# Kernel tuning notes

Hardware: AMD Instinct MI355X
Metric: run time of the kernel (lower is better)

## Reference

```python
import jax, jax.numpy as jnp
import numpy as np

N = 16000; E = 256000; K = 4000; H = 4; D = 128; CL = 16
NODE_VOCAB = 512; TASK_VOCAB = 128; NEG = 0.2


def _gat_sparse(h_in, src, dst, W, a_s, a_d, b):
    # PyG GATConv, heads=H, concat=False, eval mode (attention dropout off)
    n = h_in.shape[0]
    h = (h_in @ W.T).reshape(n, H, D)                       # [N,H,D]
    e = jax.nn.leaky_relu((h * a_s).sum(-1)[src] + (h * a_d).sum(-1)[dst], NEG)  # [E,H]
    emax = jax.ops.segment_max(e, dst, num_segments=n)
    ex = jnp.exp(e - emax[dst])
    den = jax.ops.segment_sum(ex, dst, num_segments=n)
    alpha = ex / (den[dst] + 1e-16)                         # edge softmax over dst
    out = jax.ops.segment_sum(h[src] * alpha[:, :, None], dst, num_segments=n)
    return out.mean(axis=1) + b                             # mean over heads + bias


def reference(x, edge_index, batch, task, node_emb, task_emb,
              W1, as1, ad1, b1, W2, as2, ad2, b2, W3, as3, ad3, b3,
              sag_wrel, sag_brel, sag_wroot, dmon_w, dmon_b,
              Wt, att_s_t, att_d_t, bt, gate_w, gate_b, trans_w, trans_b,
              task_w, task_b, fuse_w, fuse_b, out_w, out_b):
    src0, dst0 = edge_index[0], edge_index[1]
    loops = jnp.arange(N, dtype=src0.dtype)                 # GATConv add_self_loops=True
    src = jnp.concatenate([src0, loops]); dst = jnp.concatenate([dst0, loops])
    h = node_emb[x]
    h = jax.nn.relu(_gat_sparse(h, src, dst, W1, as1, ad1, b1))
    h = jax.nn.relu(_gat_sparse(h, src, dst, W2, as2, ad2, b2))
    h = jax.nn.relu(_gat_sparse(h, src, dst, W3, as3, ad3, b3))
    # SAGPooling: GraphConv score (add-aggr) + top-k (single graph, k=K), tanh gating
    agg = jax.ops.segment_sum(h[src0], dst0, num_segments=N)
    score = (agg @ sag_wrel.T + sag_brel + h @ sag_wroot.T)[:, 0]
    vals, perm = jax.lax.top_k(score, K)
    xp = h[perm] * jnp.tanh(vals)[:, None]                  # [K,D]
    # filter_adj + to_dense_adj: dense [K,K] adjacency among kept nodes (adj[src,dst]+=1)
    new_idx = jnp.full((N,), -1, jnp.int32).at[perm].set(jnp.arange(K, dtype=jnp.int32))
    ni, nj = new_idx[src0], new_idx[dst0]
    valid = (ni >= 0) & (nj >= 0)
    adj = jnp.zeros((K + 1, K + 1), xp.dtype).at[
        jnp.where(valid, ni, K), jnp.where(valid, nj, K)].add(1.0)[:K, :K]
    dx, adj = xp[None], adj[None]                           # [1,K,D], [1,K,K]; mask all-true
    # DMoNPooling
    s = jax.nn.softmax(dx @ dmon_w.T + dmon_b, axis=-1)     # [1,K,CL]
    out_x = jax.nn.selu(jnp.einsum('bnc,bnf->bcf', s, dx))  # [1,CL,D]
    out_adj = jnp.einsum('bnc,bnm,bmd->bcd', s, adj, s)     # [1,CL,CL]
    deg = adj.sum(axis=1)[..., None]                        # einsum('ijk->ik'): [1,K,1]
    m = deg.sum(axis=(1, 2)) / 2
    ca = jnp.einsum('bnc,bnl->bcl', s, deg)                 # [1,CL,1]
    cb = jnp.einsum('bln,bnc->blc', jnp.swapaxes(deg, 1, 2), s)  # [1,1,CL]
    spectral = (-jnp.trace(out_adj - ca @ cb / 2 / m[:, None, None], axis1=1, axis2=2) / 2 / m).mean()
    ss = jnp.einsum('bnc,bnd->bcd', s, s)
    i_s = jnp.eye(CL, dtype=ss.dtype)
    ortho = jnp.linalg.norm(ss / jnp.linalg.norm(ss, axis=(1, 2), keepdims=True)
                            - i_s / jnp.sqrt(jnp.asarray(CL, ss.dtype)), axis=(1, 2)).mean()
    cluster = (jnp.linalg.norm(s.sum(axis=1), axis=1) / K * jnp.sqrt(jnp.asarray(CL, ss.dtype)) - 1).mean()
    gp_loss = spectral + ortho + cluster
    out_adj = out_adj * (1.0 - i_s)                         # zero diagonal
    ds = jnp.sqrt(out_adj.sum(axis=2)) + 1e-15              # [1,CL]
    out_adj = out_adj / ds[:, None, :] / ds[:, :, None]
    # DenseGATConv (add_loop=True sets diag to 1; adj only used as a mask)
    hh = (out_x @ Wt.T).reshape(1, CL, H, D)
    al = jax.nn.leaky_relu((hh * att_s_t).sum(-1)[:, None, :, :]
                           + (hh * att_d_t).sum(-1)[:, :, None, :], NEG)  # [1,i,j,H]
    adj_l = out_adj * (1.0 - i_s) + i_s
    al = jnp.where(adj_l[..., None] == 0, -jnp.inf, al)
    al = jax.nn.softmax(al, axis=2)
    dg = jax.nn.relu(jnp.einsum('bijh,bjhd->bihd', al, hh).mean(axis=2) + bt)  # [1,CL,D]
    # gated readout (DenseAggregation)
    gate = jax.nn.softmax((dg @ gate_w.T + gate_b)[..., 0], axis=-1)           # [1,CL]
    ro = jnp.einsum('bn,bnd->bd', gate, dg @ trans_w.T + trans_b)              # [1,D]
    te = jax.nn.relu(task_emb[task] @ task_w.T + task_b)                       # [1,D]
    fuse = jax.nn.relu(jnp.concatenate([ro, te], axis=-1) @ fuse_w.T + fuse_b)
    out = fuse @ out_w.T + out_b                                               # [1,1]
    return out, gp_loss


def setup_inputs() -> dict:
    key = jax.random.key(0)
    ks = iter(jax.random.split(key, 64))
    def nrm(shape, scale=0.05):
        return jax.random.normal(next(ks), shape, jnp.float32) * scale
    inp = {}
    inp['x'] = jax.random.randint(next(ks), (N,), 0, NODE_VOCAB, dtype=jnp.int32)
    src = jax.random.randint(next(ks), (E,), 0, N, dtype=jnp.int32)
    off = jax.random.randint(next(ks), (E,), 1, N, dtype=jnp.int32)
    inp['edge_index'] = jnp.stack([src, (src + off) % N])  # no self-loops
    inp['batch'] = jnp.zeros((N,), jnp.int32)
    inp['task'] = jax.random.randint(next(ks), (1,), 0, TASK_VOCAB, dtype=jnp.int32)
    inp['node_emb'] = nrm((NODE_VOCAB, D), D ** -0.5)
    inp['task_emb'] = nrm((TASK_VOCAB, D), D ** -0.5)
    for i in (1, 2, 3):
        inp[f'W{i}'] = nrm((H * D, D)); inp[f'as{i}'] = nrm((H, D))
        inp[f'ad{i}'] = nrm((H, D)); inp[f'b{i}'] = jnp.zeros((D,), jnp.float32)
    inp['sag_wrel'] = nrm((1, D)); inp['sag_brel'] = jnp.zeros((1,), jnp.float32)
    inp['sag_wroot'] = nrm((1, D))
    inp['dmon_w'] = nrm((CL, D)); inp['dmon_b'] = jnp.zeros((CL,), jnp.float32)
    inp['Wt'] = nrm((H * D, D)); inp['att_s_t'] = nrm((H, D)); inp['att_d_t'] = nrm((H, D))
    inp['bt'] = jnp.zeros((D,), jnp.float32)
    inp['gate_w'] = nrm((1, D)); inp['gate_b'] = jnp.zeros((1,), jnp.float32)
    inp['trans_w'] = nrm((D, D)); inp['trans_b'] = jnp.zeros((D,), jnp.float32)
    inp['task_w'] = nrm((D, D)); inp['task_b'] = jnp.zeros((D,), jnp.float32)
    inp['fuse_w'] = nrm((D, 2 * D)); inp['fuse_b'] = jnp.zeros((D,), jnp.float32)
    inp['out_w'] = nrm((1, D)); inp['out_b'] = jnp.zeros((1,), jnp.float32)
    return inp
```

## Files before the change

kernel.cpp:

```cpp
#include <hip/hip_runtime.h>
#include <hip/hip_bf16.h>
#include <math.h>

constexpr int NN  = 16000;
constexpr int NE  = 256000;
constexpr int NET = NE + NN;
constexpr int NK  = 4000;
constexpr int NCL = 16;

constexpr int A_ADJ    = 0;
constexpr int A_SS     = 256;
constexpr int A_CSUM   = 512;
constexpr int A_V      = 528;
constexpr int A_DEGSUM = 544;
constexpr int A_OUTX   = 560;
constexpr int ACC_FLOATS = 3072;

typedef short sh8 __attribute__((ext_vector_type(8)));
typedef float f32x4 __attribute__((ext_vector_type(4)));

__device__ inline unsigned fkey(float f){
  unsigned u = __float_as_uint(f);
  return (u & 0x80000000u) ? ~u : (u | 0x80000000u);
}
__device__ inline unsigned short f2bf(float f){
  unsigned u = __float_as_uint(f);
  unsigned r = u + 0x7FFFu + ((u>>16)&1u);
  return (unsigned short)(r>>16);
}
__device__ inline float bflo(unsigned v){ return __uint_as_float(v<<16); }
__device__ inline float bfhi(unsigned v){ return __uint_as_float(v & 0xFFFF0000u); }

__global__ __launch_bounds__(256) void k_init(int* cnt, int* node2k, float* tbuf,
                       float* deg, float* acc,
                       const float* __restrict__ dw, unsigned short* __restrict__ dwb,
                       const float* __restrict__ W0, const float* __restrict__ as0, const float* __restrict__ ad0,
                       const float* __restrict__ W1, const float* __restrict__ as1, const float* __restrict__ ad1,
                       const float* __restrict__ W2, const float* __restrict__ as2, const float* __restrict__ ad2,
                       const float* __restrict__ Wt, unsigned short* __restrict__ Wtb,
                       float* __restrict__ usd, unsigned short* __restrict__ Blay){
  int i = blockIdx.x*blockDim.x + threadIdx.x;
  int stride = gridDim.x*blockDim.x;
  for (int j=i; j<NN; j+=stride){ cnt[j]=0; node2k[j]=-1; }
  for (int j=i; j<NK*NCL; j+=stride) tbuf[j]=0.f;
  for (int j=i; j<NK; j+=stride) deg[j]=0.f;
  for (int j=i; j<ACC_FLOATS; j+=stride) acc[j]=0.f;
  int b = blockIdx.x;
  const float* Wl[3] = {W0, W1, W2};
  const float* al_s[3] = {as0, as1, as2};
  const float* al_d[3] = {ad0, ad1, ad2};
  if (b < 96){
    int layer = b>>5;
    const float* W = Wl[layer];
    int idx = (b&31)*256 + threadIdx.x;
    int lane = idx&63, kc = (idx>>6)&15, c = idx>>10;
    int d = c*16 + (lane&15), q = lane>>4;
    sh8 v;
    #pragma unroll
    for (int j=0;j<8;j++){
      int kkg = kc*32 + q*8 + j;
      int h = kkg>>7, k = kkg&127;
      v[j] = (short)f2bf(W[(size_t)(h*128+d)*128 + k]);
    }
    *((sh8*)(Blay + (size_t)layer*65536 + (size_t)idx*8)) = v;
  } else if (b < 99){
    int layer = b-96;
    const float* W = Wl[layer];
    const float* as_ = al_s[layer];
    const float* ad_ = al_d[layer];
    for (int t2 = threadIdx.x; t2 < 512; t2 += 256){
      int h = t2>>7, k = t2&127;
      float ss=0.f, sd=0.f;
      for (int d=0; d<128; d++){
        float w = W[(size_t)(h*128+d)*128 + k];
        ss += as_[h*128+d]*w;
        sd += ad_[h*128+d]*w;
      }
      usd[layer*1024 + t2] = ss;
      usd[layer*1024 + 512 + t2] = sd;
    }
  } else if (b == 99){
    int idx = threadIdx.x;
    int kc = idx>>6, lane = idx&63;
    int c = lane&15, q = lane>>4;
    sh8 v;
    #pragma unroll
    for (int j=0;j<8;j++) v[j] = (short)f2bf(dw[(size_t)c*128 + kc*32 + q*8 + j]);
    ((sh8*)dwb)[idx] = v;
  } else if (b < 132){
    int idx = (b-100)*256 + threadIdx.x;
    int lane = idx&63, kc = (idx>>6)&3, ntile = idx>>8;
    int o = ntile*16 + (lane&15), q = lane>>4;
    sh8 v;
    #pragma unroll
    for (int j=0;j<8;j++) v[j] = (short)f2bf(Wt[(size_t)o*128 + kc*32 + q*8 + j]);
    ((sh8*)Wtb)[idx] = v;
  }
}

__global__ void k_count(const int* __restrict__ ei, int* __restrict__ cnt){
  int e = blockIdx.x*blockDim.x + threadIdx.x;
  if (e >= NET) return;
  int d = (e < NE) ? ei[NE+e] : (e-NE);
  atomicAdd(&cnt[d], 1);
}

__global__ __launch_bounds__(1024) void k_scan(int* cnt, int* ptr, int* fill){
  __shared__ int sums[1024];
  int t = threadIdx.x;
  constexpr int PER = 16;
  int base = t*PER;
  int v[PER];
  int run = 0;
  #pragma unroll
  for (int i=0;i<PER;i++){
    int idx = base+i;
    int c = (idx<NN)? cnt[idx] : 0;
    v[i] = run; run += c;
  }
  sums[t] = run;
  __syncthreads();
  for (int o=1;o<1024;o<<=1){
    int add = (t>=o)? sums[t-o] : 0;
    __syncthreads();
    sums[t] += add;
    __syncthreads();
  }
  int ex = sums[t] - run;
  #pragma unroll
  for (int i=0;i<PER;i++){
    int idx = base+i;
    if (idx<NN){ int p = ex+v[i]; ptr[idx]=p; fill[idx]=p; }
  }
  if (t==1023) ptr[NN]=sums[1023];
}

__global__ void k_fill(const int* __restrict__ ei, int* cur, int* csrc){
  int e = blockIdx.x*blockDim.x + threadIdx.x;
  if (e >= NET) return;
  int s, d;
  if (e < NE){ s = ei[e]; d = ei[NE+e]; } else { s = e-NE; d = e-NE; }
  int pos = atomicAdd(&cur[d], 1);
  csrc[pos] = s;
}

__global__ __launch_bounds__(64) void k_embsum(const int* __restrict__ x,
    const float* __restrict__ emb, const float* __restrict__ usd,
    unsigned short* __restrict__ hbf, float* __restrict__ sum_s,
    float* __restrict__ sum_d){
  int n = blockIdx.x, lane = threadIdx.x;
  int xv = x[n];
  float2 v = *(const float2*)&emb[(size_t)xv*128 + 2*lane];
  *(ushort2*)&hbf[(size_t)n*128 + 2*lane] = (ushort2){f2bf(v.x), f2bf(v.y)};
  float ps[4], pd[4];
  #pragma unroll
  for (int h=0;h<4;h++){
    float2 us = *(const float2*)&usd[h*128 + 2*lane];
    float2 ud = *(const float2*)&usd[512 + h*128 + 2*lane];
    ps[h] = v.x*us.x + v.y*us.y;
    pd[h] = v.x*ud.x + v.y*ud.y;
  }
  #pragma unroll
  for (int o=32;o>0;o>>=1){
    #pragma unroll
    for (int h=0;h<4;h++){ ps[h]+=__shfl_down(ps[h],o); pd[h]+=__shfl_down(pd[h],o); }
  }
  if (lane==0){
    ((float4*)sum_s)[n] = (float4){ps[0],ps[1],ps[2],ps[3]};
    ((float4*)sum_d)[n] = (float4){pd[0],pd[1],pd[2],pd[3]};
  }
}

__global__ __launch_bounds__(64) void k_edgeagg(const int* __restrict__ ptr,
    const int* __restrict__ csrc,
    const float* __restrict__ sum_s, const float* __restrict__ sum_d,
    const unsigned short* __restrict__ hbf, unsigned short* __restrict__ agg){
  __shared__ float alf[64*4];
  __shared__ int   sN[64];
  int n = blockIdx.x; int lane = threadIdx.x;
  int b0 = ptr[n], b1 = ptr[n+1];
  int deg = b1 - b0;
  float4 sd = ((const float4*)sum_d)[n];
  bool act = lane < deg;
  int s0i = -1;
  float vx=-1e30f, vy=-1e30f, vz=-1e30f, vw=-1e30f;
  if (act){
    s0i = csrc[b0+lane];
    float4 ss = ((const float4*)sum_s)[s0i];
    vx = ss.x+sd.x; vx = vx>0.f? vx : 0.2f*vx;
    vy = ss.y+sd.y; vy = vy>0.f? vy : 0.2f*vy;
    vz = ss.z+sd.z; vz = vz>0.f? vz : 0.2f*vz;
    vw = ss.w+sd.w; vw = vw>0.f? vw : 0.2f*vw;
  }
  float mx=vx, my=vy, mz=vz, mw=vw;
  for (int base=64; base<deg; base+=64){
    int j = b0+base+lane;
    if (j<b1){
      float4 ss = ((const float4*)sum_s)[csrc[j]];
      float t0=ss.x+sd.x; t0=t0>0.f?t0:0.2f*t0; mx=fmaxf(mx,t0);
      float t1=ss.y+sd.y; t1=t1>0.f?t1:0.2f*t1; my=fmaxf(my,t1);
      float t2=ss.z+sd.z; t2=t2>0.f?t2:0.2f*t2; mz=fmaxf(mz,t2);
      float t3=ss.w+sd.w; t3=t3>0.f?t3:0.2f*t3; mw=fmaxf(mw,t3);
    }
  }
  #pragma unroll
  for (int o=1;o<64;o<<=1){
    mx=fmaxf(mx,__shfl_xor(mx,o)); my=fmaxf(my,__shfl_xor(my,o));
    mz=fmaxf(mz,__shfl_xor(mz,o)); mw=fmaxf(mw,__shfl_xor(mw,o));
  }
  float dx = act? __expf(vx-mx):0.f, dy = act? __expf(vy-my):0.f;
  float dz = act? __expf(vz-mz):0.f, dw = act? __expf(vw-mw):0.f;
  for (int base=64; base<deg; base+=64){
    int j = b0+base+lane;
    if (j<b1){
      float4 ss = ((const float4*)sum_s)[csrc[j]];
      float t0=ss.x+sd.x; t0=t0>0.f?t0:0.2f*t0; dx+=__expf(t0-mx);
      float t1=ss.y+sd.y; t1=t1>0.f?t1:0.2f*t1; dy+=__expf(t1-my);
      float t2=ss.z+sd.z; t2=t2>0.f?t2:0.2f*t2; dz+=__expf(t2-mz);
      float t3=ss.w+sd.w; t3=t3>0.f?t3:0.2f*t3; dw+=__expf(t3-mw);
    }
  }
  #pragma unroll
  for (int o=1;o<64;o<<=1){
    dx+=__shfl_xor(dx,o); dy+=__shfl_xor(dy,o);
    dz+=__shfl_xor(dz,o); dw+=__shfl_xor(dw,o);
  }
  float scx = 0.25f/(dx+1e-16f), scy = 0.25f/(dy+1e-16f);
  float scz = 0.25f/(dz+1e-16f), scw = 0.25f/(dw+1e-16f);
  float a00=0.f,a01=0.f,a10=0.f,a11=0.f,a20=0.f,a21=0.f,a30=0.f,a31=0.f;
  for (int base=0; base<deg; base+=64){
    if (base){
      __syncthreads();
      int j = b0+base+lane;
      if (j<b1){
        s0i = csrc[j];
        float4 ss = ((const float4*)sum_s)[s0i];
        vx=ss.x+sd.x; vx=vx>0.f?vx:0.2f*vx;
        vy=ss.y+sd.y; vy=vy>0.f?vy:0.2f*vy;
        vz=ss.z+sd.z; vz=vz>0.f?vz:0.2f*vz;
        vw=ss.w+sd.w; vw=vw>0.f?vw:0.2f*vw;
      }
    }
    if (base+lane < deg){
      alf[lane*4+0]=__expf(vx-mx)*scx; alf[lane*4+1]=__expf(vy-my)*scy;
      alf[lane*4+2]=__expf(vz-mz)*scz; alf[lane*4+3]=__expf(vw-mw)*scw;
      sN[lane]=s0i;
    }
    __syncthreads();
    int m = deg-base; if (m>64) m=64;
    int e=0;
    for (; e+4<=m; e+=4){
      int t0=sN[e], t1=sN[e+1], t2=sN[e+2], t3=sN[e+3];
      float4 A0=*(float4*)&alf[e*4],   A1=*(float4*)&alf[e*4+4];
      float4 A2=*(float4*)&alf[e*4+8], A3=*(float4*)&alf[e*4+12];
      unsigned g0=*(const unsigned*)&hbf[(size_t)t0*128+2*lane];
      unsigned g1=*(const unsigned*)&hbf[(size_t)t1*128+2*lane];
      unsigned g2=*(const unsigned*)&hbf[(size_t)t2*128+2*lane];
      unsigned g3=*(const unsigned*)&hbf[(size_t)t3*128+2*lane];
      float p0=bflo(g0), p1=bfhi(g0);
      a00+=A0.x*p0; a01+=A0.x*p1; a10+=A0.y*p0; a11+=A0.y*p1;
      a20+=A0.z*p0; a21+=A0.z*p1; a30+=A0.w*p0; a31+=A0.w*p1;
      p0=bflo(g1); p1=bfhi(g1);
      a00+=A1.x*p0; a01+=A1.x*p1; a10+=A1.y*p0; a11+=A1.y*p1;
      a20+=A1.z*p0; a21+=A1.z*p1; a30+=A1.w*p0; a31+=A1.w*p1;
      p0=bflo(g2); p1=bfhi(g2);
      a00+=A2.x*p0; a01+=A2.x*p1; a10+=A2.y*p0; a11+=A2.y*p1;
      a20+=A2.z*p0; a21+=A2.z*p1; a30+=A2.w*p0; a31+=A2.w*p1;
      p0=bflo(g3); p1=bfhi(g3);
      a00+=A3.x*p0; a01+=A3.x*p1; a10+=A3.y*p0; a11+=A3.y*p1;
      a20+=A3.z*p0; a21+=A3.z*p1; a30+=A3.w*p0; a31+=A3.w*p1;
    }
    for (; e<m; e++){
      int t0=sN[e];
      float4 A0=*(float4*)&alf[e*4];
      unsigned g0=*(const unsigned*)&hbf[(size_t)t0*128+2*lane];
      float p0=bflo(g0), p1=bfhi(g0);
      a00+=A0.x*p0; a01+=A0.x*p1; a10+=A0.y*p0; a11+=A0.y*p1;
      a20+=A0.z*p0; a21+=A0.z*p1; a30+=A0.w*p0; a31+=A0.w*p1;
    }
  }
  unsigned short* o = agg + (size_t)n*512;
  *(ushort2*)&o[      2*lane] = (ushort2){f2bf(a00), f2bf(a01)};
  *(ushort2*)&o[128 + 2*lane] = (ushort2){f2bf(a10), f2bf(a11)};
  *(ushort2*)&o[256 + 2*lane] = (ushort2){f2bf(a20), f2bf(a21)};
  *(ushort2*)&o[384 + 2*lane] = (ushort2){f2bf(a30), f2bf(a31)};
}

__global__ __launch_bounds__(256) void k_gemmb(const unsigned short* __restrict__ A,
      const unsigned short* __restrict__ B, const float* __restrict__ bias,
      float* __restrict__ C, unsigned short* __restrict__ Cb, int writeF32,
      int mode, const float* __restrict__ usdn,
      const float* __restrict__ wrel, const float* __restrict__ wroot,
      float* __restrict__ sum_s, float* __restrict__ sum_d,
      float* __restrict__ pbuf, float* __restrict__ qbuf){
  __shared__ float U[1024];
  int tid = threadIdx.x;
  if (mode==0){
    for (int i=tid;i<1024;i+=256) U[i]=usdn[i];
  } else {
    if (tid<128) U[tid]=wrel[tid];
    else if (tid<256) U[tid]=wroot[tid-128];
  }
  __syncthreads();
  int w = tid>>6, lane = tid&63;
  int m0 = blockIdx.x*64 + w*16;
  int quad = lane>>4, col16 = lane&15;
  int mrow = m0 + col16;
  const sh8* arow = (const sh8*)(A + (size_t)mrow*512 + quad*8);
  sh8 af[16];
  #pragma unroll
  for (int kc=0;kc<16;kc++) af[kc] = arow[kc*4];
  f32x4 acc[8];
  #pragma unroll
  for (int c=0;c<8;c++) acc[c] = (f32x4){0.f,0.f,0.f,0.f};
  const sh8* bp = (const sh8*)B;
  #pragma unroll
  for (int kc=0;kc<16;kc++){
    #pragma unroll
    for (int c=0;c<8;c++){
      sh8 bf = bp[(c*16+kc)*64 + lane];
      acc[c] = __builtin_amdgcn_mfma_f32_16x16x32_bf16(af[kc], bf, acc[c], 0, 0, 0);
    }
  }
  float br[8];
  #pragma unroll
  for (int c=0;c<8;c++) br[c] = bias[c*16+col16];
  #pragma unroll
  for (int r=0;r<4;r++){
    int m = m0 + quad*4 + r;
    float vv[8];
    #pragma unroll
    for (int c=0;c<8;c++){
      vv[c] = fmaxf(acc[c][r] + br[c], 0.f);
      Cb[(size_t)m*128 + c*16+col16] = f2bf(vv[c]);
      if (writeF32) C[(size_t)m*128 + c*16+col16] = vv[c];
    }
    if (mode==0){
      float p0=0,p1=0,p2=0,p3=0,q0=0,q1=0,q2=0,q3=0;
      #pragma unroll
      for (int c=0;c<8;c++){
        int o = c*16+col16;
        float val = vv[c];
        p0+=val*U[o];     p1+=val*U[128+o]; p2+=val*U[256+o]; p3+=val*U[384+o];
        q0+=val*U[512+o]; q1+=val*U[640+o]; q2+=val*U[768+o]; q3+=val*U[896+o];
      }
      #pragma unroll
      for (int o2=1;o2<16;o2<<=1){
        p0+=__shfl_xor(p0,o2); p1+=__shfl_xor(p1,o2); p2+=__shfl_xor(p2,o2); p3+=__shfl_xor(p3,o2);
        q0+=__shfl_xor(q0,o2); q1+=__shfl_xor(q1,o2); q2+=__shfl_xor(q2,o2); q3+=__shfl_xor(q3,o2);
      }
      if (col16==0){
        ((float4*)sum_s)[m] = (float4){p0,p1,p2,p3};
        ((float4*)sum_d)[m] = (float4){q0,q1,q2,q3};
      }
    } else {
      float pp=0.f, qq=0.f;
      #pragma unroll
      for (int c=0;c<8;c++){
        int o = c*16+col16;
        pp += vv[c]*U[o]; qq += vv[c]*U[128+o];
      }
      #pragma unroll
      for (int o2=1;o2<16;o2<<=1){ pp+=__shfl_xor(pp,o2); qq+=__shfl_xor(qq,o2); }
      if (col16==0){ pbuf[m]=pp; qbuf[m]=qq; }
    }
  }
}

__global__ __launch_bounds__(64) void k_sagw(const int* __restrict__ ptr,
                           const int* __restrict__ csrc,
                           const float* __restrict__ p, const float* __restrict__ q,
                           const float* __restrict__ brel, float* __restrict__ score){
  int n = blockIdx.x; int lane = threadIdx.x;
  int b0=ptr[n], b1=ptr[n+1];
  float s=0.f;
  for (int j=b0+lane; j<b1; j+=64){
    int sj=csrc[j];
    if (sj!=n) s+=p[sj];
  }
  #pragma unroll
  for (int o=32;o>0;o>>=1) s += __shfl_down(s,o);
  if (lane==0) score[n] = s + q[n] + brel[0];
}

__global__ __launch_bounds__(1024) void k_topk(const float* __restrict__ score,
                                               int* __restrict__ sel){
  __shared__ int hist[8*257];
  __shared__ int hmerge[256];
  __shared__ unsigned sh_prefix;
  __shared__ int sh_rem;
  __shared__ int cntGT, cntEQ;
  __shared__ int ties[256];
  int t = threadIdx.x;
  int lane = t & 63;
  int rep = t >> 7;
  unsigned keys[16];
  #pragma unroll
  for (int j=0;j<16;j++){
    int i = t + j*1024;
    keys[j] = (i<NN) ? fkey(score[i]) : 0u;
  }
  if (t==0){ sh_prefix=0u; sh_rem=NK; cntGT=0; cntEQ=0; }
  __syncthreads();
  for (int p=0;p<4;p++){
    int shift = 24-8*p;
    for (int i=t;i<8*257;i+=1024) hist[i]=0;
    __syncthreads();
    unsigned prefix = sh_prefix;
    #pragma unroll
    for (int j=0;j<16;j++){
      bool val = (j<15) || (t < (NN - 15*1024));
      unsigned u = keys[j];
      bool ok = val && ((p==0) || ((u>>(shift+8)) == (prefix>>(shift+8))));
      int b = (int)((u>>shift)&255u);
      unsigned long long act = __ballot(ok);
      if (act){
        int leader = (int)(__ffsll((long long)act)-1);
        int bl = __shfl(b, leader);
        unsigned long long same = __ballot(ok && b==bl);
        if (same==act){
          if (lane==leader) atomicAdd(&hist[rep*257+bl], (int)__popcll(act));
        } else if (ok){
          atomicAdd(&hist[rep*257+b], 1);
        }
      }
    }
    __syncthreads();
    if (t<256){
      int v=0;
      #pragma unroll
      for (int r=0;r<8;r++) v += hist[r*257+t];
      hmerge[t]=v;
    }
    __syncthreads();
    if (t<64){
      int l = t;
      int b0 = 4*(63-l);
      int c3 = hmerge[b0+3], c2 = hmerge[b0+2], c1 = hmerge[b0+1], c0 = hmerge[b0];
      int gs = c0+c1+c2+c3;
      int incl = gs;
      #pragma unroll
      for (int o=1;o<64;o<<=1){
        int v = __shfl_up(incl, o);
        if (l>=o) incl += v;
      }
      int excl = incl - gs;
      int rem = sh_rem;
      int rl = rem - excl;
      if (rl > 0 && rl <= gs){
        unsigned pre = sh_prefix;
        if (rl > c3){ rl -= c3;
          if (rl > c2){ rl -= c2;
            if (rl > c1){ rl -= c1;
              sh_prefix = pre | ((unsigned)b0<<shift);     sh_rem = rl;
            } else { sh_prefix = pre | ((unsigned)(b0+1)<<shift); sh_rem = rl; }
          } else { sh_prefix = pre | ((unsigned)(b0+2)<<shift);   sh_rem = rl; }
        } else { sh_prefix = pre | ((unsigned)(b0+3)<<shift);     sh_rem = rl; }
      }
    }
    __syncthreads();
  }
  unsigned Tu = sh_prefix;
  #pragma unroll
  for (int j=0;j<16;j++){
    int i = t + j*1024;
    bool val = (i<NN);
    unsigned u = keys[j];
    bool g = val && (u>Tu), e = val && (u==Tu);
    unsigned long long mg = __ballot(g);
    if (mg){
      int leader = (int)(__ffsll((long long)mg)-1);
      int base = 0;
      if (lane==leader) base = atomicAdd(&cntGT, (int)__popcll(mg));
      base = __shfl(base, leader);
      if (g){
        int pos = base + (int)__popcll(mg & ((1ull<<lane)-1ull));
        sel[pos] = i;
      }
    }
    unsigned long long me = __ballot(e);
    if (me){
      int leader = (int)(__ffsll((long long)me)-1);
      int base = 0;
      if (lane==leader) base = atomicAdd(&cntEQ, (int)__popcll(me));
      base = __shfl(base, leader);
      if (e){
        int pos = base + (int)__popcll(me & ((1ull<<lane)-1ull));
        if (pos<256) ties[pos] = i;
      }
    }
  }
  __syncthreads();
  if (t==0){
    int base=cntGT, rem=sh_rem, nt=min(cntEQ,256);
    for (int r=0;r<rem;r++){
      int best=0x7fffffff, bi=-1;
      for (int q2=0;q2<nt;q2++){ int v=ties[q2]; if (v>=0 && v<best){best=v;bi=q2;} }
      sel[base+r] = (bi>=0)? best : 0;
      if (bi>=0) ties[bi]=-1;
    }
  }
}

__global__ __launch_bounds__(256) void k_gassign(const int* __restrict__ sel,
                          const float* __restrict__ score,
                          const float* __restrict__ h, float* __restrict__ xp,
// ... 242 lines not shown
    }
  }
  __syncthreads();
  {
    int w = t>>6, lane = t&63;
    int quad = lane>>4, col = lane&15;
    sh8 af2[2];
    #pragma unroll
    for (int kc=0;kc<2;kc++) af2[kc] = *(const sh8*)&albf[col*64 + kc*32 + quad*8];
    #pragma unroll
    for (int nt2=0; nt2<2; nt2++){
      int ntile = w*2 + nt2;
      int d = ntile*16 + col;
      f32x4 a2 = (f32x4){0.f,0.f,0.f,0.f};
      #pragma unroll
      for (int kc=0;kc<2;kc++){
        sh8 bf;
        #pragma unroll
        for (int j2=0;j2<8;j2++){
          int k = kc*32 + quad*8 + j2;
          int h2 = k>>4, jj = k&15;
          bf[j2] = (short)hhb[jj*512 + h2*128 + d];
        }
        a2 = __builtin_amdgcn_mfma_f32_16x16x32_bf16(af2[kc], bf, a2, 0, 0, 0);
      }
      float bd = bt[d];
      #pragma unroll
      for (int r=0;r<4;r++){
        int i = quad*4 + r;
        dg[i*128 + d] = fmaxf(0.25f*a2[r] + bd, 0.f);
      }
    }
  }
  __syncthreads();
  if (t<16){
    float s=0.f;
    const float4* d4 = (const float4*)&dg[t*128];
    const float4* g4 = (const float4*)gate_w;
    #pragma unroll
    for (int k2=0;k2<32;k2++){
      float4 a = d4[k2], b = g4[k2];
      s += a.x*b.x + a.y*b.y + a.z*b.z + a.w*b.w;
    }
    red[t] = s + gate_b[0];
  }
  __syncthreads();
  if (t<16){
    float mx=-1e30f; for (int i=0;i<16;i++) mx=fmaxf(mx,red[i]);
    float s=0.f; for (int i=0;i<16;i++) s+=__expf(red[i]-mx);
    gate[t]=__expf(red[t]-mx)/s;
  }
  __syncthreads();
  if (t<128){
    float s=0.f;
    for (int i=0;i<16;i++) s += gate[i]*dg[i*128+t];
    gvec[t]=s;
  }
  __syncthreads();
  if (t<128){
    float s=0.f;
    const float4* tw = (const float4*)(trans_w + (size_t)t*128);
    const float4* gv = (const float4*)gvec;
    #pragma unroll
    for (int k2=0;k2<32;k2++){
      float4 a = gv[k2], b = tw[k2];
      s += a.x*b.x + a.y*b.y + a.z*b.z + a.w*b.w;
    }
    ro[t]=s+trans_b[t];
    int tk = task[0];
    const float4* te4 = (const float4*)(task_emb + (size_t)tk*128);
    const float4* tw2 = (const float4*)(task_w + (size_t)t*128);
    float s2=0.f;
    #pragma unroll
    for (int k2=0;k2<32;k2++){
      float4 a = te4[k2], b = tw2[k2];
      s2 += a.x*b.x + a.y*b.y + a.z*b.z + a.w*b.w;
    }
    te[t]=fmaxf(s2+task_b[t],0.f);
  }
  __syncthreads();
  if (t<128){
    float s=0.f;
    const float4* fw = (const float4*)(fuse_w + (size_t)t*256);
    const float4* ro4 = (const float4*)ro;
    const float4* te4 = (const float4*)te;
    #pragma unroll
    for (int k2=0;k2<32;k2++){
      float4 a = ro4[k2], b = fw[k2];
      s += a.x*b.x + a.y*b.y + a.z*b.z + a.w*b.w;
    }
    #pragma unroll
    for (int k2=0;k2<32;k2++){
      float4 a = te4[k2], b = fw[32+k2];
      s += a.x*b.x + a.y*b.y + a.z*b.z + a.w*b.w;
    }
    fu[t]=fmaxf(s+fuse_b[t],0.f);
  }
  __syncthreads();
  float v = (t<128)? fu[t]*out_w[t] : 0.f;
  red[t]=v; __syncthreads();
  for (int o=128;o>0;o>>=1){ if (t<o) red[t]+=red[t+o]; __syncthreads(); }
  if (t==0) dout[0]=red[0]+out_b[0];
}

extern "C" void kernel_launch(void* const* d_in, const int* in_sizes, int n_in,
                              void* d_out, int out_size, void* d_ws, size_t ws_size,
                              hipStream_t stream){
  const int* x        = (const int*)d_in[0];
  const int* ei       = (const int*)d_in[1];
  const int* task     = (const int*)d_in[3];
  const float* node_emb = (const float*)d_in[4];
  const float* task_emb = (const float*)d_in[5];
  const float* W[3]  = {(const float*)d_in[6],  (const float*)d_in[10], (const float*)d_in[14]};
  const float* As_[3]= {(const float*)d_in[7],  (const float*)d_in[11], (const float*)d_in[15]};
  const float* Ad_[3]= {(const float*)d_in[8],  (const float*)d_in[12], (const float*)d_in[16]};
  const float* Bb[3] = {(const float*)d_in[9],  (const float*)d_in[13], (const float*)d_in[17]};
  const float* wrel  = (const float*)d_in[18];
  const float* brel  = (const float*)d_in[19];
  const float* wroot = (const float*)d_in[20];
  const float* dmon_w= (const float*)d_in[21];
  const float* dmon_b= (const float*)d_in[22];
  const float* Wt    = (const float*)d_in[23];
  const float* att_s = (const float*)d_in[24];
  const float* att_d = (const float*)d_in[25];
  const float* btb   = (const float*)d_in[26];
  const float* gate_w= (const float*)d_in[27];
  const float* gate_b= (const float*)d_in[28];
  const float* trans_w=(const float*)d_in[29];
  const float* trans_b=(const float*)d_in[30];
  const float* task_w= (const float*)d_in[31];
  const float* task_b= (const float*)d_in[32];
  const float* fuse_w= (const float*)d_in[33];
  const float* fuse_b= (const float*)d_in[34];
  const float* out_w = (const float*)d_in[35];
  const float* out_b = (const float*)d_in[36];
  float* dout = (float*)d_out;
  (void)in_sizes; (void)n_in; (void)out_size; (void)ws_size;

  char* base = (char*)d_ws;
  size_t off = 0;
  auto alloc = [&](size_t bytes)->char*{
    off = (off + 255) & ~(size_t)255;
    char* r = base + off; off += bytes; return r;
  };
  int* csr_ptr  = (int*)alloc((size_t)(NN+1)*4);
  int* csr_fill = (int*)alloc((size_t)NN*4);
  int* csr_src  = (int*)alloc((size_t)NET*4);
  int* sel      = (int*)alloc((size_t)NK*4);
  int* node2k   = (int*)alloc((size_t)NN*4);
  float* score  = (float*)alloc((size_t)NN*4);
  float* pbuf   = (float*)alloc((size_t)NN*4);
  float* qbuf   = (float*)alloc((size_t)NN*4);
  float* h_a    = (float*)alloc((size_t)NN*128*4);
  unsigned short* hbf  = (unsigned short*)alloc((size_t)NN*128*2);
  unsigned short* aggb = (unsigned short*)alloc((size_t)NN*512*2);
  unsigned short* blay = (unsigned short*)alloc((size_t)3*65536*2);
  unsigned short* dwb  = (unsigned short*)alloc((size_t)256*8*2);
  unsigned short* wtb  = (unsigned short*)alloc((size_t)65536*2);
  float* usd    = (float*)alloc((size_t)3*1024*4);
  float* sum_s  = (float*)alloc((size_t)NN*4*4);
  float* sum_d  = (float*)alloc((size_t)NN*4*4);
  float* xp     = (float*)alloc((size_t)NK*128*4);
  float* sA     = (float*)alloc((size_t)NK*16*4);
  float* tbuf   = (float*)alloc((size_t)NK*16*4);
  float* deg    = (float*)alloc((size_t)NK*4);
  float* acc    = (float*)alloc((size_t)ACC_FLOATS*4);

  k_init<<<256, 256, 0, stream>>>(csr_fill, node2k, tbuf, deg, acc, dmon_w, dwb,
                                  W[0], As_[0], Ad_[0], W[1], As_[1], Ad_[1],
                                  W[2], As_[2], Ad_[2], Wt, wtb, usd, blay);
  k_count<<<(NET+255)/256, 256, 0, stream>>>(ei, csr_fill);
  k_scan<<<1, 1024, 0, stream>>>(csr_fill, csr_ptr, csr_fill);
  k_fill<<<(NET+255)/256, 256, 0, stream>>>(ei, csr_fill, csr_src);
  k_embsum<<<NN, 64, 0, stream>>>(x, node_emb, usd, hbf, sum_s, sum_d);

  for (int l=0;l<3;l++){
    k_edgeagg<<<NN, 64, 0, stream>>>(csr_ptr, csr_src, sum_s, sum_d, hbf, aggb);
    if (l<2){
      k_gemmb<<<NN/64, 256, 0, stream>>>(aggb, blay + (size_t)l*65536, Bb[l],
                                         h_a, hbf, 0, 0, usd + (l+1)*1024,
                                         nullptr, nullptr, sum_s, sum_d,
                                         nullptr, nullptr);
    } else {
      k_gemmb<<<NN/64, 256, 0, stream>>>(aggb, blay + (size_t)2*65536, Bb[2],
                                         h_a, hbf, 1, 1, nullptr,
                                         wrel, wroot, nullptr, nullptr,
                                         pbuf, qbuf);
    }
  }
  k_sagw<<<NN, 64, 0, stream>>>(csr_ptr, csr_src, pbuf, qbuf, brel, score);
  k_topk<<<1, 1024, 0, stream>>>(score, sel);
  k_gassign<<<NK/16, 256, 0, stream>>>(sel, score, h_a, xp, node2k, dwb, dmon_b, sA);
  k_edgepool<<<(NE+255)/256, 256, 0, stream>>>(ei, node2k, sA, tbuf, deg);
  k_pool<<<P_BLOCKS, 256, 0, stream>>>(sA, xp, tbuf, deg, acc);
  k_tail<<<1, 256, 0, stream>>>(acc, wtb, att_s, att_d, btb, gate_w, gate_b,
                                trans_w, trans_b, task, task_emb, task_w, task_b,
                                fuse_w, fuse_b, out_w, out_b, dout);
}
```

Before: 413.5 us.

## Fuse GAT edge aggregation into per-layer MFMA GEMM kernel via LDS staging

Merges the per-node attention softmax/aggregation kernel with the following bf16 MFMA projection GEMM. Each 256-thread block aggregates 64 nodes into shared memory and then runs the GEMM from LDS, which removes the global write and read of the 16000x512 aggregate buffer. The node features and attention sums now ping-pong between two buffers to avoid read/write races across blocks. Attention weights are broadcast with wave shuffles instead of LDS. The trade-off is far fewer blocks (250) with serial 16-node loops per wave and a large LDS footprint, which reduces the latency hiding available to the irregular gather.

```diff
diff --git a/kernel.cpp b/kernel.cpp
--- a/kernel.cpp
+++ b/kernel.cpp
@@ -171,145 +171,142 @@
   }
 }
 
-__global__ __launch_bounds__(64) void k_edgeagg(const int* __restrict__ ptr,
-    const int* __restrict__ csrc,
-    const float* __restrict__ sum_s, const float* __restrict__ sum_d,
-    const unsigned short* __restrict__ hbf, unsigned short* __restrict__ agg){
-  __shared__ float alf[64*4];
-  __shared__ int   sN[64];
-  int n = blockIdx.x; int lane = threadIdx.x;
-  int b0 = ptr[n], b1 = ptr[n+1];
-  int deg = b1 - b0;
-  float4 sd = ((const float4*)sum_d)[n];
-  bool act = lane < deg;
-  int s0i = -1;
-  float vx=-1e30f, vy=-1e30f, vz=-1e30f, vw=-1e30f;
-  if (act){
-    s0i = csrc[b0+lane];
-    float4 ss = ((const float4*)sum_s)[s0i];
-    vx = ss.x+sd.x; vx = vx>0.f? vx : 0.2f*vx;
-    vy = ss.y+sd.y; vy = vy>0.f? vy : 0.2f*vy;
-    vz = ss.z+sd.z; vz = vz>0.f? vz : 0.2f*vz;
-    vw = ss.w+sd.w; vw = vw>0.f? vw : 0.2f*vw;
-  }
-  float mx=vx, my=vy, mz=vz, mw=vw;
-  for (int base=64; base<deg; base+=64){
-    int j = b0+base+lane;
-    if (j<b1){
-      float4 ss = ((const float4*)sum_s)[csrc[j]];
-      float t0=ss.x+sd.x; t0=t0>0.f?t0:0.2f*t0; mx=fmaxf(mx,t0);
-      float t1=ss.y+sd.y; t1=t1>0.f?t1:0.2f*t1; my=fmaxf(my,t1);
-      float t2=ss.z+sd.z; t2=t2>0.f?t2:0.2f*t2; mz=fmaxf(mz,t2);
-      float t3=ss.w+sd.w; t3=t3>0.f?t3:0.2f*t3; mw=fmaxf(mw,t3);
-    }
-  }
-  #pragma unroll
-  for (int o=1;o<64;o<<=1){
-    mx=fmaxf(mx,__shfl_xor(mx,o)); my=fmaxf(my,__shfl_xor(my,o));
-    mz=fmaxf(mz,__shfl_xor(mz,o)); mw=fmaxf(mw,__shfl_xor(mw,o));
-  }
-  float dx = act? __expf(vx-mx):0.f, dy = act? __expf(vy-my):0.f;
-  float dz = act? __expf(vz-mz):0.f, dw = act? __expf(vw-mw):0.f;
-  for (int base=64; base<deg; base+=64){
-    int j = b0+base+lane;
-    if (j<b1){
-      float4 ss = ((const float4*)sum_s)[csrc[j]];
-      float t0=ss.x+sd.x; t0=t0>0.f?t0:0.2f*t0; dx+=__expf(t0-mx);
-      float t1=ss.y+sd.y; t1=t1>0.f?t1:0.2f*t1; dy+=__expf(t1-my);
-      float t2=ss.z+sd.z; t2=t2>0.f?t2:0.2f*t2; dz+=__expf(t2-mz);
-      float t3=ss.w+sd.w; t3=t3>0.f?t3:0.2f*t3; dw+=__expf(t3-mw);
-    }
-  }
-  #pragma unroll
-  for (int o=1;o<64;o<<=1){
-    dx+=__shfl_xor(dx,o); dy+=__shfl_xor(dy,o);
-    dz+=__shfl_xor(dz,o); dw+=__shfl_xor(dw,o);
-  }
-  float scx = 0.25f/(dx+1e-16f), scy = 0.25f/(dy+1e-16f);
-  float scz = 0.25f/(dz+1e-16f), scw = 0.25f/(dw+1e-16f);
-  float a00=0.f,a01=0.f,a10=0.f,a11=0.f,a20=0.f,a21=0.f,a30=0.f,a31=0.f;
-  for (int base=0; base<deg; base+=64){
-    if (base){
-      __syncthreads();
-      int j = b0+base+lane;
-      if (j<b1){
-        s0i = csrc[j];
-        float4 ss = ((const float4*)sum_s)[s0i];
-        vx=ss.x+sd.x; vx=vx>0.f?vx:0.2f*vx;
-        vy=ss.y+sd.y; vy=vy>0.f?vy:0.2f*vy;
-        vz=ss.z+sd.z; vz=vz>0.f?vz:0.2f*vz;
-        vw=ss.w+sd.w; vw=vw>0.f?vw:0.2f*vw;
-      }
-    }
-    if (base+lane < deg){
-      alf[lane*4+0]=__expf(vx-mx)*scx; alf[lane*4+1]=__expf(vy-my)*scy;
-      alf[lane*4+2]=__expf(vz-mz)*scz; alf[lane*4+3]=__expf(vw-mw)*scw;
-      sN[lane]=s0i;
-    }
-    __syncthreads();
-    int m = deg-base; if (m>64) m=64;
-    int e=0;
-    for (; e+4<=m; e+=4){
-      int t0=sN[e], t1=sN[e+1], t2=sN[e+2], t3=sN[e+3];
-      float4 A0=*(float4*)&alf[e*4],   A1=*(float4*)&alf[e*4+4];
-      float4 A2=*(float4*)&alf[e*4+8], A3=*(float4*)&alf[e*4+12];
-      unsigned g0=*(const unsigned*)&hbf[(size_t)t0*128+2*lane];
-      unsigned g1=*(const unsigned*)&hbf[(size_t)t1*128+2*lane];
-      unsigned g2=*(const unsigned*)&hbf[(size_t)t2*128+2*lane];
-      unsigned g3=*(const unsigned*)&hbf[(size_t)t3*128+2*lane];
-      float p0=bflo(g0), p1=bfhi(g0);
-      a00+=A0.x*p0; a01+=A0.x*p1; a10+=A0.y*p0; a11+=A0.y*p1;
-      a20+=A0.z*p0; a21+=A0.z*p1; a30+=A0.w*p0; a31+=A0.w*p1;
-      p0=bflo(g1); p1=bfhi(g1);
-      a00+=A1.x*p0; a01+=A1.x*p1; a10+=A1.y*p0; a11+=A1.y*p1;
-      a20+=A1.z*p0; a21+=A1.z*p1; a30+=A1.w*p0; a31+=A1.w*p1;
-      p0=bflo(g2); p1=bfhi(g2);
-      a00+=A2.x*p0; a01+=A2.x*p1; a10+=A2.y*p0; a11+=A2.y*p1;
-      a20+=A2.z*p0; a21+=A2.z*p1; a30+=A2.w*p0; a31+=A2.w*p1;
-      p0=bflo(g3); p1=bfhi(g3);
-      a00+=A3.x*p0; a01+=A3.x*p1; a10+=A3.y*p0; a11+=A3.y*p1;
-      a20+=A3.z*p0; a21+=A3.z*p1; a30+=A3.w*p0; a31+=A3.w*p1;
-    }
-    for (; e<m; e++){
-      int t0=sN[e];
-      float4 A0=*(float4*)&alf[e*4];
-      unsigned g0=*(const unsigned*)&hbf[(size_t)t0*128+2*lane];
-      float p0=bflo(g0), p1=bfhi(g0);
-      a00+=A0.x*p0; a01+=A0.x*p1; a10+=A0.y*p0; a11+=A0.y*p1;
-      a20+=A0.z*p0; a21+=A0.z*p1; a30+=A0.w*p0; a31+=A0.w*p1;
-    }
-  }
-  unsigned short* o = agg + (size_t)n*512;
-  *(ushort2*)&o[      2*lane] = (ushort2){f2bf(a00), f2bf(a01)};
-  *(ushort2*)&o[128 + 2*lane] = (ushort2){f2bf(a10), f2bf(a11)};
-  *(ushort2*)&o[256 + 2*lane] = (ushort2){f2bf(a20), f2bf(a21)};
-  *(ushort2*)&o[384 + 2*lane] = (ushort2){f2bf(a30), f2bf(a31)};
-}
-
-__global__ __launch_bounds__(256) void k_gemmb(const unsigned short* __restrict__ A,
+constexpr int AL_STR = 520;
+__global__ __launch_bounds__(256) void k_layer(const int* __restrict__ ptr,
+      const int* __restrict__ csrc,
+      const float* __restrict__ sum_s_in, const float* __restrict__ sum_d_in,
+      const unsigned short* __restrict__ hb_in,
       const unsigned short* __restrict__ B, const float* __restrict__ bias,
-      float* __restrict__ C, unsigned short* __restrict__ Cb, int writeF32,
+      unsigned short* __restrict__ hb_out, float* __restrict__ C, int writeF32,
       int mode, const float* __restrict__ usdn,
       const float* __restrict__ wrel, const float* __restrict__ wroot,
-      float* __restrict__ sum_s, float* __restrict__ sum_d,
+      float* __restrict__ sum_s_out, float* __restrict__ sum_d_out,
       float* __restrict__ pbuf, float* __restrict__ qbuf){
+  __shared__ unsigned short aggL[64*AL_STR];
   __shared__ float U[1024];
   int tid = threadIdx.x;
+  int w = tid>>6, lane = tid&63;
+  int n0 = blockIdx.x*64;
   if (mode==0){
     for (int i=tid;i<1024;i+=256) U[i]=usdn[i];
   } else {
     if (tid<128) U[tid]=wrel[tid];
     else if (tid<256) U[tid]=wroot[tid-128];
   }
-  __syncthreads();
-  int w = tid>>6, lane = tid&63;
-  int m0 = blockIdx.x*64 + w*16;
+  for (int k=0;k<16;k++){
+    int n = n0 + w*16 + k;
+    int b0 = ptr[n], b1 = ptr[n+1];
+    int deg = b1 - b0;
+    float4 sd = ((const float4*)sum_d_in)[n];
+    bool act = lane < deg;
+    int sidx = 0;
+    float vx=-1e30f, vy=-1e30f, vz=-1e30f, vw=-1e30f;
+    if (act){
+      sidx = csrc[b0+lane];
+      float4 ss = ((const float4*)sum_s_in)[sidx];
+      vx = ss.x+sd.x; vx = vx>0.f? vx : 0.2f*vx;
+      vy = ss.y+sd.y; vy = vy>0.f? vy : 0.2f*vy;
+      vz = ss.z+sd.z; vz = vz>0.f? vz : 0.2f*vz;
+      vw = ss.w+sd.w; vw = vw>0.f? vw : 0.2f*vw;
+    }
+    float mx=vx, my=vy, mz=vz, mw=vw;
+    for (int base=64; base<deg; base+=64){
+      int j = b0+base+lane;
+      if (j<b1){
+        float4 ss = ((const float4*)sum_s_in)[csrc[j]];
+        float t0=ss.x+sd.x; t0=t0>0.f?t0:0.2f*t0; mx=fmaxf(mx,t0);
+        float t1=ss.y+sd.y; t1=t1>0.f?t1:0.2f*t1; my=fmaxf(my,t1);
+        float t2=ss.z+sd.z; t2=t2>0.f?t2:0.2f*t2; mz=fmaxf(mz,t2);
+        float t3=ss.w+sd.w; t3=t3>0.f?t3:0.2f*t3; mw=fmaxf(mw,t3);
+      }
+    }
+    #pragma unroll
+    for (int o=1;o<64;o<<=1){
+      mx=fmaxf(mx,__shfl_xor(mx,o)); my=fmaxf(my,__shfl_xor(my,o));
+      mz=fmaxf(mz,__shfl_xor(mz,o)); mw=fmaxf(mw,__shfl_xor(mw,o));
+    }
+    float dx = act? __expf(vx-mx):0.f, dy = act? __expf(vy-my):0.f;
+    float dz = act? __expf(vz-mz):0.f, dw = act? __expf(vw-mw):0.f;
+    for (int base=64; base<deg; base+=64){
+      int j = b0+base+lane;
+      if (j<b1){
+        float4 ss = ((const float4*)sum_s_in)[csrc[j]];
+        float t0=ss.x+sd.x; t0=t0>0.f?t0:0.2f*t0; dx+=__expf(t0-mx);
+        float t1=ss.y+sd.y; t1=t1>0.f?t1:0.2f*t1; dy+=__expf(t1-my);
+        float t2=ss.z+sd.z; t2=t2>0.f?t2:0.2f*t2; dz+=__expf(t2-mz);
+        float t3=ss.w+sd.w; t3=t3>0.f?t3:0.2f*t3; dw+=__expf(t3-mw);
+      }
+    }
+    #pragma unroll
+    for (int o=1;o<64;o<<=1){
+      dx+=__shfl_xor(dx,o); dy+=__shfl_xor(dy,o);
+      dz+=__shfl_xor(dz,o); dw+=__shfl_xor(dw,o);
+    }
+    float scx = 0.25f/(dx+1e-16f), scy = 0.25f/(dy+1e-16f);
+    float scz = 0.25f/(dz+1e-16f), scw = 0.25f/(dw+1e-16f);
+    float a00=0.f,a01=0.f,a10=0.f,a11=0.f,a20=0.f,a21=0.f,a30=0.f,a31=0.f;
+    for (int base=0; base<deg; base+=64){
+      if (base){
+        int j = b0+base+lane;
+        if (j<b1){
+          sidx = csrc[j];
+          float4 ss = ((const float4*)sum_s_in)[sidx];
+          vx=ss.x+sd.x; vx=vx>0.f?vx:0.2f*vx;
+          vy=ss.y+sd.y; vy=vy>0.f?vy:0.2f*vy;
+          vz=ss.z+sd.z; vz=vz>0.f?vz:0.2f*vz;
+          vw=ss.w+sd.w; vw=vw>0.f?vw:0.2f*vw;
+        }
+      }
+      float ax = __expf(vx-mx)*scx, ay = __expf(vy-my)*scy;
+      float az = __expf(vz-mz)*scz, aw = __expf(vw-mw)*scw;
+      int m = deg-base; if (m>64) m=64;
+      int e=0;
+      for (; e+4<=m; e+=4){
+        int t0=__shfl(sidx,e),   t1=__shfl(sidx,e+1);
+        int t2=__shfl(sidx,e+2), t3=__shfl(sidx,e+3);
+        float A0x=__shfl(ax,e),   A0y=__shfl(ay,e),   A0z=__shfl(az,e),   A0w=__shfl(aw,e);
+        float A1x=__shfl(ax,e+1), A1y=__shfl(ay,e+1), A1z=__shfl(az,e+1), A1w=__shfl(aw,e+1);
+        float A2x=__shfl(ax,e+2), A2y=__shfl(ay,e+2), A2z=__shfl(az,e+2), A2w=__shfl(aw,e+2);
+        float A3x=__shfl(ax,e+3), A3y=__shfl(ay,e+3), A3z=__shfl(az,e+3), A3w=__shfl(aw,e+3);
+        unsigned g0=*(const unsigned*)&hb_in[(size_t)t0*128+2*lane];
+        unsigned g1=*(const unsigned*)&hb_in[(size_t)t1*128+2*lane];
+        unsigned g2=*(const unsigned*)&hb_in[(size_t)t2*128+2*lane];
+        unsigned g3=*(const unsigned*)&hb_in[(size_t)t3*128+2*lane];
+        float p0=bflo(g0), p1=bfhi(g0);
+        a00+=A0x*p0; a01+=A0x*p1; a10+=A0y*p0; a11+=A0y*p1;
+        a20+=A0z*p0; a21+=A0z*p1; a30+=A0w*p0; a31+=A0w*p1;
+        p0=bflo(g1); p1=bfhi(g1);
+        a00+=A1x*p0; a01+=A1x*p1; a10+=A1y*p0; a11+=A1y*p1;
+        a20+=A1z*p0; a21+=A1z*p1; a30+=A1w*p0; a31+=A1w*p1;
+        p0=bflo(g2); p1=bfhi(g2);
+        a00+=A2x*p0; a01+=A2x*p1; a10+=A2y*p0; a11+=A2y*p1;
+        a20+=A2z*p0; a21+=A2z*p1; a30+=A2w*p0; a31+=A2w*p1;
+        p0=bflo(g3); p1=bfhi(g3);
+        a00+=A3x*p0; a01+=A3x*p1; a10+=A3y*p0; a11+=A3y*p1;
+        a20+=A3z*p0; a21+=A3z*p1; a30+=A3w*p0; a31+=A3w*p1;
+      }
+      for (; e<m; e++){
+        int t0=__shfl(sidx,e);
+        float A0x=__shfl(ax,e), A0y=__shfl(ay,e), A0z=__shfl(az,e), A0w=__shfl(aw,e);
+        unsigned g0=*(const unsigned*)&hb_in[(size_t)t0*128+2*lane];
+        float p0=bflo(g0), p1=bfhi(g0);
+        a00+=A0x*p0; a01+=A0x*p1; a10+=A0y*p0; a11+=A0y*p1;
+        a20+=A0z*p0; a21+=A0z*p1; a30+=A0w*p0; a31+=A0w*p1;
+      }
+    }
+    unsigned short* o = &aggL[(w*16+k)*AL_STR];
+    *(ushort2*)&o[      2*lane] = (ushort2){f2bf(a00), f2bf(a01)};
+    *(ushort2*)&o[128 + 2*lane] = (ushort2){f2bf(a10), f2bf(a11)};
+    *(ushort2*)&o[256 + 2*lane] = (ushort2){f2bf(a20), f2bf(a21)};
+    *(ushort2*)&o[384 + 2*lane] = (ushort2){f2bf(a30), f2bf(a31)};
+  }
+  __syncthreads();
+  int m0 = n0 + w*16;
   int quad = lane>>4, col16 = lane&15;
-  int mrow = m0 + col16;
-  const sh8* arow = (const sh8*)(A + (size_t)mrow*512 + quad*8);
+  int lrow = w*16 + col16;
   sh8 af[16];
   #pragma unroll
-  for (int kc=0;kc<16;kc++) af[kc] = arow[kc*4];
+  for (int kc=0;kc<16;kc++) af[kc] = *(const sh8*)&aggL[lrow*AL_STR + kc*32 + quad*8];
   f32x4 acc[8];
   #pragma unroll
   for (int c=0;c<8;c++) acc[c] = (f32x4){0.f,0.f,0.f,0.f};
@@ -332,7 +329,7 @@
     #pragma unroll
     for (int c=0;c<8;c++){
       vv[c] = fmaxf(acc[c][r] + br[c], 0.f);
-      Cb[(size_t)m*128 + c*16+col16] = f2bf(vv[c]);
+      hb_out[(size_t)m*128 + c*16+col16] = f2bf(vv[c]);
       if (writeF32) C[(size_t)m*128 + c*16+col16] = vv[c];
     }
     if (mode==0){
@@ -350,8 +347,8 @@
         q0+=__shfl_xor(q0,o2); q1+=__shfl_xor(q1,o2); q2+=__shfl_xor(q2,o2); q3+=__shfl_xor(q3,o2);
       }
       if (col16==0){
-        ((float4*)sum_s)[m] = (float4){p0,p1,p2,p3};
-        ((float4*)sum_d)[m] = (float4){q0,q1,q2,q3};
+        ((float4*)sum_s_out)[m] = (float4){p0,p1,p2,p3};
+        ((float4*)sum_d_out)[m] = (float4){q0,q1,q2,q3};
       }
     } else {
       float pp=0.f, qq=0.f;
@@ -900,14 +897,16 @@
   float* pbuf   = (float*)alloc((size_t)NN*4);
   float* qbuf   = (float*)alloc((size_t)NN*4);
   float* h_a    = (float*)alloc((size_t)NN*128*4);
-  unsigned short* hbf  = (unsigned short*)alloc((size_t)NN*128*2);
-  unsigned short* aggb = (unsigned short*)alloc((size_t)NN*512*2);
+  unsigned short* hb0 = (unsigned short*)alloc((size_t)NN*128*2);
+  unsigned short* hb1 = (unsigned short*)alloc((size_t)NN*128*2);
   unsigned short* blay = (unsigned short*)alloc((size_t)3*65536*2);
   unsigned short* dwb  = (unsigned short*)alloc((size_t)256*8*2);
   unsigned short* wtb  = (unsigned short*)alloc((size_t)65536*2);
   float* usd    = (float*)alloc((size_t)3*1024*4);
-  float* sum_s  = (float*)alloc((size_t)NN*4*4);
-  float* sum_d  = (float*)alloc((size_t)NN*4*4);
+  float* ss0    = (float*)alloc((size_t)NN*4*4);
+  float* sd0    = (float*)alloc((size_t)NN*4*4);
+  float* ss1    = (float*)alloc((size_t)NN*4*4);
+  float* sd1    = (float*)alloc((size_t)NN*4*4);
   float* xp     = (float*)alloc((size_t)NK*128*4);
   float* sA     = (float*)alloc((size_t)NK*16*4);
   float* tbuf   = (float*)alloc((size_t)NK*16*4);
@@ -920,22 +919,21 @@
   k_count<<<(NET+255)/256, 256, 0, stream>>>(ei, csr_fill);
   k_scan<<<1, 1024, 0, stream>>>(csr_fill, csr_ptr, csr_fill);
   k_fill<<<(NET+255)/256, 256, 0, stream>>>(ei, csr_fill, csr_src);
-  k_embsum<<<NN, 64, 0, stream>>>(x, node_emb, usd, hbf, sum_s, sum_d);
-
-  for (int l=0;l<3;l++){
-    k_edgeagg<<<NN, 64, 0, stream>>>(csr_ptr, csr_src, sum_s, sum_d, hbf, aggb);
-    if (l<2){
-      k_gemmb<<<NN/64, 256, 0, stream>>>(aggb, blay + (size_t)l*65536, Bb[l],
-                                         h_a, hbf, 0, 0, usd + (l+1)*1024,
-                                         nullptr, nullptr, sum_s, sum_d,
-                                         nullptr, nullptr);
-    } else {
-      k_gemmb<<<NN/64, 256, 0, stream>>>(aggb, blay + (size_t)2*65536, Bb[2],
-                                         h_a, hbf, 1, 1, nullptr,
-                                         wrel, wroot, nullptr, nullptr,
-                                         pbuf, qbuf);
-    }
-  }
+  k_embsum<<<NN, 64, 0, stream>>>(x, node_emb, usd, hb0, ss0, sd0);
+
+  k_layer<<<NN/64, 256, 0, stream>>>(csr_ptr, csr_src, ss0, sd0, hb0,
+                                     blay, Bb[0], hb1, nullptr, 0,
+                                     0, usd + 1024, nullptr, nullptr,
+                                     ss1, sd1, nullptr, nullptr);
+  k_layer<<<NN/64, 256, 0, stream>>>(csr_ptr, csr_src, ss1, sd1, hb1,
+                                     blay + 65536, Bb[1], hb0, nullptr, 0,
+                                     0, usd + 2048, nullptr, nullptr,
+                                     ss0, sd0, nullptr, nullptr);
+  k_layer<<<NN/64, 256, 0, stream>>>(csr_ptr, csr_src, ss0, sd0, hb0,
+                                     blay + 2*65536, Bb[2], hb1, h_a, 1,
+                                     1, nullptr, wrel, wroot,
+                                     nullptr, nullptr, pbuf, qbuf);
+
   k_sagw<<<NN, 64, 0, stream>>>(csr_ptr, csr_src, pbuf, qbuf, brel, score);
   k_topk<<<1, 1024, 0, stream>>>(score, sel);
   k_gassign<<<NK/16, 256, 0, stream>>>(sel, score, h_a, xp, node2k, dwb, dmon_b, sA);
```

Result: slower. 517.8 us (+25.2%).
